# Optimization experiments

Measured on AMD Instinct MI355X. Metric: run time of the kernel, lower is better.

## Reference

```python
import math
import jax, jax.numpy as jnp
import numpy as np

B, S, D_IN, D_OUT = 8, 4096, 512, 512
CHUNK = 64
MAX_LR = 0.2        # config.max_memory_lr
MIN_DECAY = 0.5     # config.min_memory_decay
MAX_NORM = 30.0     # config.memory_max_norm
NORM_EPS = 1e-5     # config.norm_eps (used in normalize_for_delta)


def setup_inputs() -> dict:
    key = jax.random.key(0)
    ks = jax.random.split(key, 5)
    x = jax.random.normal(ks[0], (B, S, D_IN), dtype=jnp.float32)
    # M_init: xavier_uniform(gain=0.1) ~ small; use small normal
    M_init = jax.random.normal(ks[1], (D_OUT, D_IN), dtype=jnp.float32) * 0.02
    # hyperparam projections (Linear(d_in, 1)); torch init: zero weight, logit bias.
    # Use small random weights so the data-dependent path is exercised.
    eta_w = jax.random.normal(ks[2], (1, D_IN), dtype=jnp.float32) * 0.01
    eta_b = jnp.full((1,), math.log(0.08 / 0.92), dtype=jnp.float32)   # inv_sig(memory_lr_init)
    alpha_w = jax.random.normal(ks[3], (1, D_IN), dtype=jnp.float32) * 0.01
    alpha_b = jnp.full((1,), math.log(0.85 / 0.15), dtype=jnp.float32)  # inv_sig(memory_decay_init)
    gate_w = jax.random.normal(ks[4], (1, D_IN), dtype=jnp.float32) * 0.01
    gate_b = jnp.full((1,), 2.0, dtype=jnp.float32)
    return {"x": x, "M_init": M_init, "eta_w": eta_w, "eta_b": eta_b,
            "alpha_w": alpha_w, "alpha_b": alpha_b, "gate_w": gate_w, "gate_b": gate_b}


def _forward(x, M_init, eta_w, eta_b, alpha_w, alpha_b, gate_w, gate_b):
    n_chunks = S // CHUNK
    # [n_chunks, B, C, d_in] for scan over chunks
    xc = x.reshape(B, n_chunks, CHUNK, D_IN).transpose(1, 0, 2, 3)
    M0 = jnp.broadcast_to(M_init, (B, D_OUT, D_IN))

    def step(M, chunk):  # M: [B, d_out, d_in], chunk: [B, C, d_in]
        # per-chunk hyperparams (training mode: base logits = 0)
        eta_tok = jax.nn.sigmoid(chunk @ eta_w.T + eta_b) * MAX_LR            # [B,C,1]
        alpha_tok = MIN_DECAY + jax.nn.sigmoid(chunk @ alpha_w.T + alpha_b) * (1.0 - MIN_DECAY)
        eta = eta_tok.mean(axis=1, keepdims=True)    # [B,1,1]
        alpha = alpha_tok.mean(axis=1, keepdims=True)
        # retrieval: chunk @ M^T
        outputs = jnp.einsum('bcd,bod->bco', chunk, M)  # [B,C,d_out]
        # normalized keys (F.normalize: x / max(||x||, eps))
        kn = jnp.linalg.norm(chunk, axis=-1, keepdims=True)
        keys = chunk / jnp.maximum(kn, NORM_EPS)
        k_mean = keys.mean(axis=1)        # [B,d_in]
        v_target = outputs.mean(axis=1)   # [B,d_out]
        # delta rule rank-1 update
        Mk = jnp.einsum('bod,bd->bo', M, k_mean)
        error = v_target - Mk
        update = error[:, :, None] * k_mean[:, None, :]  # [B,d_out,d_in]
        # chunk_scale = min(C/chunk_size, 1) = 1 here
        M_new = alpha * M + eta * update
        gate = jax.nn.sigmoid(k_mean @ gate_w.T + gate_b)[:, :, None]  # [B,1,1]
        M_new = gate * M_new + (1.0 - gate) * M
        # frobenius-norm clamp
        M_norm = jnp.sqrt(jnp.sum(M_new * M_new, axis=(-2, -1), keepdims=True))
        scale = jnp.minimum(MAX_NORM / (M_norm + 1e-6), 1.0)
        return M_new * scale, outputs

    M_fin, outs = jax.lax.scan(step, M0, xc)  # outs: [n_chunks,B,C,d_out]
    out = outs.transpose(1, 0, 2, 3).reshape(B, S, D_OUT)
    return out, M_fin


def reference(x, M_init, eta_w, eta_b, alpha_w, alpha_b, gate_w, gate_b):
    return _forward(x, M_init, eta_w, eta_b, alpha_w, alpha_b, gate_w, gate_b)
```

## Files before the change

### kernel.cpp

```cpp
#include <hip/hip_runtime.h>
#include <math.h>

#define DIN  512
#define DOUT 512
#define CHK  64
#define NCH  64
#define NB   8
#define SEQ  4096

typedef short bh8_t __attribute__((ext_vector_type(8)));
typedef float f32x4 __attribute__((ext_vector_type(4)));

__device__ __forceinline__ float sigmoidf_(float z){ return 1.0f/(1.0f+__expf(-z)); }

__device__ __forceinline__ unsigned short f2bf(float f){
  unsigned u = __float_as_uint(f);
  unsigned r = (u + 0x7fffu + ((u>>16)&1u)) >> 16;
  return (unsigned short)r;
}
__device__ __forceinline__ void store_bf4(unsigned short* p, float4 v){
  uint2 u;
  u.x = (unsigned)f2bf(v.x) | ((unsigned)f2bf(v.y)<<16);
  u.y = (unsigned)f2bf(v.z) | ((unsigned)f2bf(v.w)<<16);
  *(uint2*)p = u;
}

__global__ __launch_bounds__(256) void k0_m0h(const float* __restrict__ M0, unsigned short* __restrict__ M0h){
  int idx = (blockIdx.x*256 + threadIdx.x)*4;
  float4 v = *(const float4*)(M0+idx);
  store_bf4(M0h+idx, v);
}

__global__ __launch_bounds__(256) void k1_stats(
    const float* __restrict__ x,
    const float* __restrict__ eta_w, const float* __restrict__ eta_b,
    const float* __restrict__ alpha_w, const float* __restrict__ alpha_b,
    const float* __restrict__ gate_w, const float* __restrict__ gate_b,
    float* __restrict__ KM, float* __restrict__ Dv, unsigned short* __restrict__ KMh,
    float* __restrict__ C1, float* __restrict__ C2, float* __restrict__ KM2, float* __restrict__ Q,
    unsigned short* __restrict__ xh)
{
  int j = blockIdx.x, b = blockIdx.y;
  const float* xc = x + ((size_t)b*SEQ + (size_t)j*CHK) * DIN;
  int tid = threadIdx.x;
  int wave = tid >> 6, lane = tid & 63;

  float km_acc[8], xb_acc[8];
#pragma unroll
  for (int k=0;k<8;k++){ km_acc[k]=0.f; xb_acc[k]=0.f; }
  float eta_sum = 0.f, alpha_sum = 0.f;
  float ew[8], aw[8];
#pragma unroll
  for (int k=0;k<8;k++){ ew[k]=eta_w[lane*8+k]; aw[k]=alpha_w[lane*8+k]; }

  for (int tt=0; tt<16; tt++){
    int t = wave*16 + tt;
    const float* xr = xc + (size_t)t*DIN + lane*8;
    float v[8];
#pragma unroll
    for (int k=0;k<8;k++) v[k]=xr[k];
    if (xh){
      uint4 hv;
      hv.x = (unsigned)f2bf(v[0]) | ((unsigned)f2bf(v[1])<<16);
      hv.y = (unsigned)f2bf(v[2]) | ((unsigned)f2bf(v[3])<<16);
      hv.z = (unsigned)f2bf(v[4]) | ((unsigned)f2bf(v[5])<<16);
      hv.w = (unsigned)f2bf(v[6]) | ((unsigned)f2bf(v[7])<<16);
      *(uint4*)&xh[((size_t)b*SEQ + (size_t)j*CHK + t)*DIN + lane*8] = hv;
    }
    float pe=0.f, pa=0.f, pn=0.f;
#pragma unroll
    for (int k=0;k<8;k++){ pe += v[k]*ew[k]; pa += v[k]*aw[k]; pn += v[k]*v[k]; }
#pragma unroll
    for (int off=32; off; off>>=1){
      pe += __shfl_xor(pe, off);
      pa += __shfl_xor(pa, off);
      pn += __shfl_xor(pn, off);
    }
    float inv = 1.0f / fmaxf(sqrtf(pn), 1e-5f);
    eta_sum   += sigmoidf_(pe + eta_b[0]);
    alpha_sum += sigmoidf_(pa + alpha_b[0]);
#pragma unroll
    for (int k=0;k<8;k++){ km_acc[k] += v[k]*inv; xb_acc[k] += v[k]; }
  }

  __shared__ float sKM[4][DIN];
  __shared__ float sXB[4][DIN];
  __shared__ float sEA[4][2];
  __shared__ float sred[4][2];
#pragma unroll
  for (int k=0;k<8;k++){ sKM[wave][lane*8+k]=km_acc[k]; sXB[wave][lane*8+k]=xb_acc[k]; }
  if (lane==0){ sEA[wave][0]=eta_sum; sEA[wave][1]=alpha_sum; }
  __syncthreads();

  float gpart=0.f, km2part=0.f;
  float kmv[2], dvv[2];
#pragma unroll
  for (int k=0;k<2;k++){
    int d = tid*2+k;
    float km = (sKM[0][d]+sKM[1][d]+sKM[2][d]+sKM[3][d]) * (1.0f/64.0f);
    float xb = (sXB[0][d]+sXB[1][d]+sXB[2][d]+sXB[3][d]) * (1.0f/64.0f);
    kmv[k]=km; dvv[k]=xb-km;
    gpart  += km * gate_w[d];
    km2part+= km * km;
  }
#pragma unroll
  for (int off=32; off; off>>=1){
    gpart   += __shfl_xor(gpart, off);
    km2part += __shfl_xor(km2part, off);
  }
  if (lane==0){ sred[wave][0]=gpart; sred[wave][1]=km2part; }
  __syncthreads();

  size_t base = ((size_t)b*NCH + j)*DIN;
#pragma unroll
  for (int k=0;k<2;k++){
    int d = tid*2+k;
    KM[base+d]=kmv[k];
    Dv[base+d]=dvv[k];
    KMh[base+d]=f2bf(kmv[k]);
  }
  if (tid==0){
    float gdot = sred[0][0]+sred[1][0]+sred[2][0]+sred[3][0];
    float km2  = sred[0][1]+sred[1][1]+sred[2][1]+sred[3][1];
    float etam = (sEA[0][0]+sEA[1][0]+sEA[2][0]+sEA[3][0]) * (1.0f/64.0f);
    float alpm = (sEA[0][1]+sEA[1][1]+sEA[2][1]+sEA[3][1]) * (1.0f/64.0f);
    float eta   = 0.2f * etam;
    float alpha = 0.5f + 0.5f * alpm;
    float gate  = sigmoidf_(gdot + gate_b[0]);
    float c1 = gate*alpha + 1.0f - gate;
    float c2 = gate*eta;
    C1[b*NCH+j]  = c1;
    C2[b*NCH+j]  = c2;
    KM2[b*NCH+j] = km2;
    Q[b*NCH+j]   = c2/c1;
  }
}

__global__ __launch_bounds__(256) void k2_g0h0(
    const float* __restrict__ KM, const float* __restrict__ Dv,
    const float* __restrict__ M0, float* __restrict__ G0, float* __restrict__ H0)
{
  int j = blockIdx.x, b = blockIdx.y, half = blockIdx.z;
  __shared__ float sD[DIN], sK[DIN];
  int tid = threadIdx.x;
  size_t base = ((size_t)b*NCH+j)*DIN;
  for (int d=tid; d<DIN; d+=256){ sD[d]=Dv[base+d]; sK[d]=KM[base+d]; }
  __syncthreads();
  int o = half*256 + tid;
  const float* mr = M0 + (size_t)o*DIN;
  float ag=0.f, ah=0.f;
  for (int d=0; d<DIN; d+=4){
    float4 m = *(const float4*)(mr+d);
    ag += m.x*sD[d] + m.y*sD[d+1] + m.z*sD[d+2] + m.w*sD[d+3];
    ah += m.x*sK[d] + m.y*sK[d+1] + m.z*sK[d+2] + m.w*sK[d+3];
  }
  G0[base+o]=ag; H0[base+o]=ah;
}

__global__ __launch_bounds__(512) void k2b_gram(
    const float* __restrict__ KM, const float* __restrict__ Dv,
    const float* __restrict__ Q,
    float* __restrict__ GT, float* __restrict__ WT)
{
  int i = blockIdx.x, b = blockIdx.y;
  __shared__ float sKi[DIN];
  int tid = threadIdx.x;
  const float* kmi = KM + ((size_t)b*NCH+i)*DIN;
  for (int d=tid; d<DIN; d+=512) sKi[d]=kmi[d];
  __syncthreads();
  float qi = Q[b*NCH+i];
  int wave = tid>>6, lane = tid&63;
  for (int j=wave; j<NCH; j+=8){
    const float* dj = Dv + ((size_t)b*NCH+j)*DIN;
    const float* kj = KM + ((size_t)b*NCH+j)*DIN;
    float pd=0.f, pk=0.f;
#pragma unroll
    for (int k=0;k<8;k++){
      int d = lane + k*64;
      pd += sKi[d]*dj[d];
      pk += sKi[d]*kj[d];
    }
#pragma unroll
    for (int off=32; off; off>>=1){ pd += __shfl_xor(pd,off); pk += __shfl_xor(pk,off); }
    if (lane==0){
      GT[((size_t)b*NCH+j)*NCH + i] = qi*pd;
      WT[((size_t)b*NCH+j)*NCH + i] = qi*pk;
    }
  }
}

__global__ __launch_bounds__(64) void k3a_rec(
    const float* __restrict__ G0, const float* __restrict__ H0,
    const float* __restrict__ GT, const float* __restrict__ WT,
    const float* __restrict__ Q,
    float* __restrict__ AU, unsigned short* __restrict__ UQTh, float* __restrict__ DOTS)
{
  int dblk = blockIdx.x, b = blockIdx.y;
  int lane = threadIdx.x;
  int d = dblk*64 + lane;

  __shared__ float sMT[NCH*NCH];
  __shared__ float sWT[NCH*NCH];
  __shared__ float sq[NCH];

  const float4* gt4 = (const float4*)&GT[(size_t)b*NCH*NCH];
  const float4* wt4 = (const float4*)&WT[(size_t)b*NCH*NCH];
#pragma unroll
  for (int t=0;t<16;t++){
    int idx4 = t*64 + lane;
    int idx  = idx4*4;
    int j = idx>>6, i0 = idx&63;
    float4 g = gt4[idx4];
    float4 w = wt4[idx4];
    if (i0+0 >= j){ g.x=0.f; w.x=0.f; }
    if (i0+1 >= j){ g.y=0.f; w.y=0.f; }
    if (i0+2 >= j){ g.z=0.f; w.z=0.f; }
    if (i0+3 >= j){ g.w=0.f; w.w=0.f; }
    *(float4*)&sMT[idx] = g;
    *(float4*)&sWT[idx] = w;
  }
  sq[lane] = Q[b*NCH+lane];
  __syncthreads();

  float au[NCH];
  size_t gb = (size_t)b*NCH*DOUT + d;
#pragma unroll
  for (int j=0;j<NCH;j++) au[j] = G0[gb + (size_t)j*DOUT];

#pragma unroll
  for (int j=1;j<NCH;j++){
    float a = au[j];
    const f32x4* row = (const f32x4*)&sMT[j*64];
    int ng = (j+3)>>2;
#pragma unroll
    for (int g=0; g<ng; g++){
      f32x4 c = row[g];
      a += c[0]*au[g*4+0] + c[1]*au[g*4+1] + c[2]*au[g*4+2] + c[3]*au[g*4+3];
    }
    au[j] = a;
  }
#pragma unroll
  for (int j=0;j<NCH;j++) AU[gb + (size_t)j*DOUT] = au[j];

#pragma unroll
  for (int g=0; g<8; g++){
    uint4 hv;
    hv.x = (unsigned)f2bf(au[g*8+0]*sq[g*8+0]) | ((unsigned)f2bf(au[g*8+1]*sq[g*8+1])<<16);
    hv.y = (unsigned)f2bf(au[g*8+2]*sq[g*8+2]) | ((unsigned)f2bf(au[g*8+3]*sq[g*8+3])<<16);
    hv.z = (unsigned)f2bf(au[g*8+4]*sq[g*8+4]) | ((unsigned)f2bf(au[g*8+5]*sq[g*8+5])<<16);
    hv.w = (unsigned)f2bf(au[g*8+6]*sq[g*8+6]) | ((unsigned)f2bf(au[g*8+7]*sq[g*8+7])<<16);
    *(uint4*)&UQTh[((size_t)b*DOUT + d)*NCH + g*8] = hv;
  }

#pragma unroll
  for (int j=0;j<NCH;j++){
    float w = H0[gb + (size_t)j*DOUT];
    const f32x4* row = (const f32x4*)&sWT[j*64];
    int ng = (j+3)>>2;
#pragma unroll
    for (int g=0; g<ng; g++){
      f32x4 c = row[g];
      w += c[0]*au[g*4+0] + c[1]*au[g*4+1] + c[2]*au[g*4+2] + c[3]*au[g*4+3];
    }
    float s1 = au[j]*w, s2 = au[j]*au[j];
#pragma unroll
    for (int off=32; off; off>>=1){ s1+=__shfl_xor(s1,off); s2+=__shfl_xor(s2,off); }
    if (lane==0){
      DOTS[(((size_t)b*8+dblk)*NCH+j)*2+0] = s1;
      DOTS[(((size_t)b*8+dblk)*NCH+j)*2+1] = s2;
    }
  }
}

__global__ __launch_bounds__(256) void k3b_chain(
    const float* __restrict__ M0, const float* __restrict__ DOTS,
    const float* __restrict__ C1, const float* __restrict__ C2, const float* __restrict__ KM2,
    float* __restrict__ P)
{
  int b = blockIdx.x;
  int tid = threadIdx.x, wave = tid>>6, lane = tid&63;
  __shared__ float sF[4];
  __shared__ float suw[NCH], suu[NCH], sc1[NCH], sc2[NCH], skm2[NCH];

  float f0p = 0.f;
  const float4* m4 = (const float4*)M0;
  for (int i=tid; i<(DOUT*DIN)/4; i+=256){
    float4 v = m4[i];
    f0p += v.x*v.x + v.y*v.y + v.z*v.z + v.w*v.w;
  }
#pragma unroll
  for (int off=32; off; off>>=1) f0p += __shfl_xor(f0p, off);
  if (lane==0) sF[wave]=f0p;

  if (tid < NCH){
    float uw=0.f, uu=0.f;
#pragma unroll
    for (int k=0;k<8;k++){
      uw += DOTS[(((size_t)b*8+k)*NCH+tid)*2+0];
      uu += DOTS[(((size_t)b*8+k)*NCH+tid)*2+1];
    }
    suw[tid]=uw; suu[tid]=uu;
    sc1[tid]=C1[b*NCH+tid]; sc2[tid]=C2[b*NCH+tid]; skm2[tid]=KM2[b*NCH+tid];
  }
  __syncthreads();

  if (tid==0){
    float F = sF[0]+sF[1]+sF[2]+sF[3];
    float p = 1.f;
    P[b*65+0] = 1.f;
    for (int j=0;j<NCH;j++){
      float uw = suw[j], uu = suu[j];
      float c1 = sc1[j], c2 = sc2[j], km2 = skm2[j];
      uw *= p*p; uu *= p*p;
      float Fnew = c1*c1*F + 2.f*c1*c2*uw + c2*c2*uu*km2;
      float scale = fminf(30.0f/(sqrtf(Fnew)+1e-6f), 1.0f);
      F = scale*scale*Fnew;
      p = scale*c1*p;
      P[b*65+j+1] = p;
    }
  }
}

__global__ __launch_bounds__(256) void k4s_s(
    const float* __restrict__ x, const unsigned short* __restrict__ xh,
    const unsigned short* __restrict__ KMh,
    unsigned short* __restrict__ Sh, int use_xh)
{
  int tt = blockIdx.x, b = blockIdx.y;
  int tid = threadIdx.x;
  int lane = tid&63, w = tid>>6, m = lane&15, q = lane>>4;
  __shared__ unsigned short As[64*72];
  __shared__ unsigned short Bs[64*72];
  f32x4 acc[4];
  f32x4 z = {0.f,0.f,0.f,0.f};
#pragma unroll
  for (int nf=0;nf<4;nf++) acc[nf]=z;

  for (int k0=0;k0<DIN;k0+=64){
    uint4 bb[2];
#pragma unroll
    for (int v=0;v<2;v++){
      int idx=v*256+tid; int il=idx>>3, cc=idx&7;
      bb[v] = *(const uint4*)&KMh[((size_t)b*NCH+il)*DIN + k0 + cc*8];
    }
    if (use_xh){
      uint4 av[2];
#pragma unroll
      for (int v=0;v<2;v++){
        int idx=v*256+tid; int row=idx>>3, cc=idx&7;
        av[v] = *(const uint4*)&xh[((size_t)b*SEQ + (size_t)tt*64 + row)*DIN + k0 + cc*8];
      }
      __syncthreads();
#pragma unroll
      for (int v=0;v<2;v++){
        int idx=v*256+tid; int row=idx>>3, cc=idx&7;
        *(uint4*)&As[row*72 + cc*8] = av[v];
      }
    } else {
      float4 xa[4];
#pragma unroll
      for (int v=0;v<4;v++){
        int idx=v*256+tid; int row=idx>>4, cc=idx&15;
        xa[v] = *(const float4*)(x + ((size_t)b*SEQ + (size_t)tt*64 + row)*DIN + k0 + cc*4);
      }
      __syncthreads();
#pragma unroll
      for (int v=0;v<4;v++){
        int idx=v*256+tid; int row=idx>>4, cc=idx&15;
        store_bf4(&As[row*72 + cc*4], xa[v]);
      }
    }
#pragma unroll
    for (int v=0;v<2;v++){
      int idx=v*256+tid; int il=idx>>3, cc=idx&7;
      *(uint4*)&Bs[il*72 + cc*8] = bb[v];
    }
    __syncthreads();
#pragma unroll
    for (int kk=0;kk<2;kk++){
      bh8_t af = *(bh8_t*)&As[(w*16+m)*72 + kk*32 + q*8];
#pragma unroll
      for (int nf=0;nf<4;nf++){
        bh8_t bf_ = *(bh8_t*)&Bs[(nf*16+m)*72 + kk*32 + q*8];
        acc[nf] = __builtin_amdgcn_mfma_f32_16x16x32_bf16(af, bf_, acc[nf], 0,0,0);
      }
    }
  }
  __syncthreads();
  unsigned short* tb = As + w*16*72;
#pragma unroll
  for (int nf=0;nf<4;nf++)
#pragma unroll
    for (int r=0;r<4;r++)
      tb[(q*4+r)*72 + nf*16 + m] = f2bf(acc[nf][r]);
#pragma unroll
  for (int v=0;v<2;v++){
    int idx = v*64 + lane;
    int row = idx>>3, c8 = idx&7;
    uint4 vv = *(uint4*)&tb[row*72 + c8*8];
    *(uint4*)&Sh[((size_t)b*SEQ + (size_t)tt*64 + w*16 + row)*NCH + c8*8] = vv;
  }
}

__global__ __launch_bounds__(256) void k4_out(
    const float* __restrict__ x, const unsigned short* __restrict__ xh,
    const unsigned short* __restrict__ M0h,
    const unsigned short* __restrict__ Sh, const unsigned short* __restrict__ UQTh,
    const float* __restrict__ P, float* __restrict__ out, int use_xh)
{
  int ot = blockIdx.x, j = blockIdx.y, b = blockIdx.z;
  int tid = threadIdx.x;
  int lane = tid&63, w = tid>>6, m = lane&15, q = lane>>4;
  int O0 = ot*128;
  __shared__ __align__(16) char pool[33792];
  unsigned short* As = (unsigned short*)pool;
  unsigned short* Bs = (unsigned short*)pool + 64*72;
  float* ep = (float*)pool;
  f32x4 acc[8];
  f32x4 z = {0.f,0.f,0.f,0.f};
#pragma unroll
  for (int nf=0;nf<8;nf++) acc[nf]=z;
  float p = P[b*65 + j];

  for (int idx=tid; idx<64*64; idx+=256){
    int t = idx>>6, i = idx&63;
    As[t*72+i] = (i<j) ? Sh[((size_t)b*SEQ + (size_t)j*64 + t)*NCH + i] : (unsigned short)0;
  }
#pragma unroll
  for (int v=0; v<4; v++){
    int idx = v*256+tid;
    int ol = idx>>3, cc = idx&7;
    *(uint4*)&Bs[ol*72 + cc*8] = *(const uint4*)&UQTh[((size_t)b*DOUT + O0+ol)*NCH + cc*8];
  }
  __syncthreads();
#pragma unroll
  for (int kk=0;kk<2;kk++){
    bh8_t af = *(bh8_t*)&As[(w*16+m)*72 + kk*32 + q*8];
#pragma unroll
    for (int nf=0;nf<8;nf++){
      bh8_t bf_ = *(bh8_t*)&Bs[(nf*16+m)*72 + kk*32 + q*8];
      acc[nf] = __builtin_amdgcn_mfma_f32_16x16x32_bf16(af, bf_, acc[nf], 0,0,0);
    }
  }

  for (int k0=0;k0<DIN;k0+=64){
    uint4 bb[4];
#pragma unroll
    for (int v=0;v<4;v++){
      int idx=v*256+tid; int ol=idx>>3, cc=idx&7;
      bb[v] = *(const uint4*)&M0h[(size_t)(O0+ol)*DIN + k0 + cc*8];
    }
    if (use_xh){
      uint4 av[2];
#pragma unroll
      for (int v=0;v<2;v++){
        int idx=v*256+tid; int row=idx>>3, cc=idx&7;
        av[v] = *(const uint4*)&xh[((size_t)b*SEQ + (size_t)j*64 + row)*DIN + k0 + cc*8];
      }
      __syncthreads();
#pragma unroll
      for (int v=0;v<2;v++){
        int idx=v*256+tid; int row=idx>>3, cc=idx&7;
        *(uint4*)&As[row*72 + cc*8] = av[v];
      }
    } else {
      float4 xa[4];
#pragma unroll
      for (int v=0;v<4;v++){
        int idx=v*256+tid; int row=idx>>4, cc=idx&15;
        xa[v] = *(const float4*)(x + ((size_t)b*SEQ + (size_t)j*64 + row)*DIN + k0 + cc*4);
      }
      __syncthreads();
#pragma unroll
      for (int v=0;v<4;v++){
        int idx=v*256+tid; int row=idx>>4, cc=idx&15;
        store_bf4(&As[row*72 + cc*4], xa[v]);
      }
    }
#pragma unroll
    for (int v=0;v<4;v++){
      int idx=v*256+tid; int ol=idx>>3, cc=idx&7;
      *(uint4*)&Bs[ol*72 + cc*8] = bb[v];
    }
    __syncthreads();
#pragma unroll
    for (int kk=0;kk<2;kk++){
      bh8_t af = *(bh8_t*)&As[(w*16+m)*72 + kk*32 + q*8];
#pragma unroll
      for (int nf=0;nf<8;nf++){
        bh8_t bf_ = *(bh8_t*)&Bs[(nf*16+m)*72 + kk*32 + q*8];
        acc[nf] = __builtin_amdgcn_mfma_f32_16x16x32_bf16(af, bf_, acc[nf], 0,0,0);
      }
    }
  }

  __syncthreads();
  float* epw = ep + w*16*132;
#pragma unroll
  for (int nf=0;nf<8;nf++)
#pragma unroll
    for (int r=0;r<4;r++)
      epw[(q*4+r)*132 + nf*16 + m] = p*acc[nf][r];
#pragma unroll
  for (int v=0;v<8;v++){
    int idx = v*64 + lane;
    int row = idx>>5, c4 = idx&31;
    float4 vv = *(float4*)&epw[row*132 + c4*4];
    *(float4*)&out[((size_t)b*SEQ + (size_t)j*64 + w*16 + row)*DOUT + O0 + c4*4] = vv;
  }
}

__global__ __launch_bounds__(256) void k5_mfin(
    const float* __restrict__ M0, const float* __restrict__ KM,
    const float* __restrict__ AU, const float* __restrict__ P, const float* __restrict__ Q,
    float* __restrict__ Mout)
{
  int ob = blockIdx.x, b = blockIdx.y;
  int tid = threadIdx.x;
  __shared__ float uo[64][8];
  for (int idx=tid; idx<512; idx+=256){
    int i = idx>>3, oo = idx&7;
    uo[i][oo] = Q[b*NCH+i] * AU[((size_t)b*NCH+i)*DOUT + ob*8+oo];
  }
  __syncthreads();
  float p64 = P[b*65+NCH];
  float acc[2][8];
#pragma unroll
  for (int h=0;h<2;h++)
#pragma unroll
    for (int oo=0;oo<8;oo++) acc[h][oo]=0.f;
  int d0 = tid, d1 = tid+256;
  for (int i=0;i<64;i++){
    float k0 = KM[((size_t)b*NCH+i)*DIN + d0];
    float k1 = KM[((size_t)b*NCH+i)*DIN + d1];
#pragma unroll
    for (int oo=0;oo<8;oo++){
      float u = uo[i][oo];
      acc[0][oo] += u*k0;
      acc[1][oo] += u*k1;
    }
  }
#pragma unroll
  for (int oo=0;oo<8;oo++){
    int o = ob*8+oo;
    Mout[((size_t)b*DOUT + o)*DIN + d0] = p64*(M0[(size_t)o*DIN+d0] + acc[0][oo]);
    Mout[((size_t)b*DOUT + o)*DIN + d1] = p64*(M0[(size_t)o*DIN+d1] + acc[1][oo]);
  }
}

extern "C" void kernel_launch(void* const* d_in, const int* in_sizes, int n_in,
                              void* d_out, int out_size, void* d_ws, size_t ws_size,
                              hipStream_t stream) {
  const float* x       = (const float*)d_in[0];
  const float* M0      = (const float*)d_in[1];
  const float* eta_w   = (const float*)d_in[2];
  const float* eta_b   = (const float*)d_in[3];
  const float* alpha_w = (const float*)d_in[4];
  const float* alpha_b = (const float*)d_in[5];
  const float* gate_w  = (const float*)d_in[6];
  const float* gate_b  = (const float*)d_in[7];
  float* out = (float*)d_out;

  float* ws = (float*)d_ws;
  float* KM   = ws;
  float* Dv   = KM   + 262144;
  float* G0   = Dv   + 262144;
  float* H0   = G0   + 262144;
  float* AU   = H0   + 262144;
  float* GT   = AU   + 262144;
  float* WT   = GT   + 32768;
  float* C1   = WT   + 32768;
  float* C2   = C1   + 512;
  float* KM2  = C2   + 512;
  float* Q    = KM2  + 512;
  float* P    = Q    + 512;
  float* DOTS = P    + 1024;
  unsigned short* M0h  = (unsigned short*)(DOTS + 8192);
  unsigned short* KMh  = M0h  + 262144;
  unsigned short* Sh   = KMh  + 262144;
  unsigned short* UQTh = Sh   + 2097152;
  unsigned short* xh   = UQTh + 262144;

  size_t base_bytes = (size_t)((char*)xh - (char*)d_ws);
  size_t need_xh = base_bytes + (size_t)16777216*2;
  int use_xh = (ws_size >= need_xh) ? 1 : 0;
  unsigned short* xh_arg = use_xh ? xh : (unsigned short*)0;

  k0_m0h<<<dim3(256), 256, 0, stream>>>(M0, M0h);
  k1_stats<<<dim3(NCH, NB), 256, 0, stream>>>(x, eta_w, eta_b, alpha_w, alpha_b,
                                              gate_w, gate_b, KM, Dv, KMh, C1, C2, KM2, Q, xh_arg);
  k2_g0h0<<<dim3(NCH, NB, 2), 256, 0, stream>>>(KM, Dv, M0, G0, H0);
  k2b_gram<<<dim3(NCH, NB), 512, 0, stream>>>(KM, Dv, Q, GT, WT);
  k4s_s<<<dim3(SEQ/64, NB), 256, 0, stream>>>(x, xh, KMh, Sh, use_xh);
  k3a_rec<<<dim3(8, NB), 64, 0, stream>>>(G0, H0, GT, WT, Q, AU, UQTh, DOTS);
  k3b_chain<<<dim3(NB), 256, 0, stream>>>(M0, DOTS, C1, C2, KM2, P);
  k4_out<<<dim3(4, NCH, NB), 256, 0, stream>>>(x, xh, M0h, Sh, UQTh, P, out, use_xh);
  k5_mfin<<<dim3(64, NB), 256, 0, stream>>>(M0, KM, AU, P, Q, out + (size_t)NB*SEQ*DOUT);
}
```

Measured before the change: 498.0 us.

## Enlarge k4_out tile to 256 rows with 2x4 wave grid per block

The output GEMM kernel now has each 512-thread block cover 256 sequence rows (four chunks) by 128 output columns instead of 64 rows. Waves are laid out on a 4x2 grid, each computing a 64x64 sub-tile, so every M0h tile loaded into LDS is reused across four times as many rows. The causal masking of the Sh coefficients moves to per-row bitmasks on vectorized loads, and the per-chunk scale P is chosen per wave row. The aim is to cut redundant M0h traffic and raise MFMA work per LDS load, at the cost of more shared memory, more registers and fewer blocks in the grid (512 instead of 2048).

```diff
diff --git a/kernel.cpp b/kernel.cpp
--- a/kernel.cpp
+++ b/kernel.cpp
@@ -402,111 +402,136 @@
   }
 }
 
-__global__ __launch_bounds__(256) void k4_out(
+__global__ __launch_bounds__(512, 4) void k4_out(
     const float* __restrict__ x, const unsigned short* __restrict__ xh,
     const unsigned short* __restrict__ M0h,
     const unsigned short* __restrict__ Sh, const unsigned short* __restrict__ UQTh,
     const float* __restrict__ P, float* __restrict__ out, int use_xh)
 {
-  int ot = blockIdx.x, j = blockIdx.y, b = blockIdx.z;
+  int ot = blockIdx.x, rb = blockIdx.y, b = blockIdx.z;
   int tid = threadIdx.x;
   int lane = tid&63, w = tid>>6, m = lane&15, q = lane>>4;
+  int wr = w>>1, wc = w&1;
   int O0 = ot*128;
-  __shared__ __align__(16) char pool[33792];
+  int R0 = rb*256;
+
+  __shared__ __align__(16) char pool[55296];
   unsigned short* As = (unsigned short*)pool;
-  unsigned short* Bs = (unsigned short*)pool + 64*72;
+  unsigned short* Bs = (unsigned short*)pool + 256*72;
   float* ep = (float*)pool;
-  f32x4 acc[8];
+
+  f32x4 acc[4][4];
   f32x4 z = {0.f,0.f,0.f,0.f};
 #pragma unroll
-  for (int nf=0;nf<8;nf++) acc[nf]=z;
-  float p = P[b*65 + j];
-
-  for (int idx=tid; idx<64*64; idx+=256){
-    int t = idx>>6, i = idx&63;
-    As[t*72+i] = (i<j) ? Sh[((size_t)b*SEQ + (size_t)j*64 + t)*NCH + i] : (unsigned short)0;
-  }
+  for (int mi=0;mi<4;mi++)
+#pragma unroll
+    for (int nf=0;nf<4;nf++) acc[mi][nf]=z;
+
 #pragma unroll
   for (int v=0; v<4; v++){
-    int idx = v*256+tid;
+    int idx = v*512 + tid;
+    int row = idx>>3, cc = idx&7;
+    int j = (R0 + row)>>6;
+    uint4 sv = *(const uint4*)&Sh[((size_t)b*SEQ + R0 + row)*NCH + cc*8];
+    int i0 = cc*8;
+    unsigned m0 = (i0+0 < j) ? ((i0+1 < j)?0xFFFFFFFFu:0x0000FFFFu) : 0u;
+    unsigned m1 = (i0+2 < j) ? ((i0+3 < j)?0xFFFFFFFFu:0x0000FFFFu) : 0u;
+    unsigned m2 = (i0+4 < j) ? ((i0+5 < j)?0xFFFFFFFFu:0x0000FFFFu) : 0u;
+    unsigned m3 = (i0+6 < j) ? ((i0+7 < j)?0xFFFFFFFFu:0x0000FFFFu) : 0u;
+    sv.x&=m0; sv.y&=m1; sv.z&=m2; sv.w&=m3;
+    *(uint4*)&As[row*72 + cc*8] = sv;
+  }
+#pragma unroll
+  for (int v=0; v<2; v++){
+    int idx = v*512 + tid;
     int ol = idx>>3, cc = idx&7;
     *(uint4*)&Bs[ol*72 + cc*8] = *(const uint4*)&UQTh[((size_t)b*DOUT + O0+ol)*NCH + cc*8];
   }
   __syncthreads();
 #pragma unroll
   for (int kk=0;kk<2;kk++){
-    bh8_t af = *(bh8_t*)&As[(w*16+m)*72 + kk*32 + q*8];
-#pragma unroll
-    for (int nf=0;nf<8;nf++){
-      bh8_t bf_ = *(bh8_t*)&Bs[(nf*16+m)*72 + kk*32 + q*8];
-      acc[nf] = __builtin_amdgcn_mfma_f32_16x16x32_bf16(af, bf_, acc[nf], 0,0,0);
+#pragma unroll
+    for (int mi=0;mi<4;mi++){
+      bh8_t af = *(bh8_t*)&As[(wr*64+mi*16+m)*72 + kk*32 + q*8];
+#pragma unroll
+      for (int nf=0;nf<4;nf++){
+        bh8_t bf_ = *(bh8_t*)&Bs[(wc*64+nf*16+m)*72 + kk*32 + q*8];
+        acc[mi][nf] = __builtin_amdgcn_mfma_f32_16x16x32_bf16(af, bf_, acc[mi][nf], 0,0,0);
+      }
     }
   }
 
   for (int k0=0;k0<DIN;k0+=64){
-    uint4 bb[4];
+    uint4 bb[2];
+#pragma unroll
+    for (int v=0;v<2;v++){
+      int idx=v*512+tid; int ol=idx>>3, cc=idx&7;
+      bb[v] = *(const uint4*)&M0h[(size_t)(O0+ol)*DIN + k0 + cc*8];
+    }
+    if (use_xh){
+      uint4 av[4];
+#pragma unroll
+      for (int v=0;v<4;v++){
+        int idx=v*512+tid; int row=idx>>3, cc=idx&7;
+        av[v] = *(const uint4*)&xh[((size_t)b*SEQ + R0 + row)*DIN + k0 + cc*8];
+      }
+      __syncthreads();
+#pragma unroll
+      for (int v=0;v<4;v++){
+        int idx=v*512+tid; int row=idx>>3, cc=idx&7;
+        *(uint4*)&As[row*72 + cc*8] = av[v];
+      }
+    } else {
+      float4 xa[8];
+#pragma unroll
+      for (int v=0;v<8;v++){
+        int idx=v*512+tid; int row=idx>>4, cc=idx&15;
+        xa[v] = *(const float4*)(x + ((size_t)b*SEQ + R0 + row)*DIN + k0 + cc*4);
+      }
+      __syncthreads();
+#pragma unroll
+      for (int v=0;v<8;v++){
+        int idx=v*512+tid; int row=idx>>4, cc=idx&15;
+        store_bf4(&As[row*72 + cc*4], xa[v]);
+      }
+    }
+#pragma unroll
+    for (int v=0;v<2;v++){
+      int idx=v*512+tid; int ol=idx>>3, cc=idx&7;
+      *(uint4*)&Bs[ol*72 + cc*8] = bb[v];
+    }
+    __syncthreads();
+#pragma unroll
+    for (int kk=0;kk<2;kk++){
+#pragma unroll
+      for (int mi=0;mi<4;mi++){
+        bh8_t af = *(bh8_t*)&As[(wr*64+mi*16+m)*72 + kk*32 + q*8];
+#pragma unroll
+        for (int nf=0;nf<4;nf++){
+          bh8_t bf_ = *(bh8_t*)&Bs[(wc*64+nf*16+m)*72 + kk*32 + q*8];
+          acc[mi][nf] = __builtin_amdgcn_mfma_f32_16x16x32_bf16(af, bf_, acc[mi][nf], 0,0,0);
+        }
+      }
+    }
+  }
+
+  __syncthreads();
+  float p = P[b*65 + rb*4 + wr];
+  float* epw = ep + w*(16*68);
+#pragma unroll
+  for (int mi=0; mi<4; mi++){
+#pragma unroll
+    for (int nf=0;nf<4;nf++)
+#pragma unroll
+      for (int r=0;r<4;r++)
+        epw[(q*4+r)*68 + nf*16 + m] = p*acc[mi][nf][r];
 #pragma unroll
     for (int v=0;v<4;v++){
-      int idx=v*256+tid; int ol=idx>>3, cc=idx&7;
-      bb[v] = *(const uint4*)&M0h[(size_t)(O0+ol)*DIN + k0 + cc*8];
-    }
-    if (use_xh){
-      uint4 av[2];
-#pragma unroll
-      for (int v=0;v<2;v++){
-        int idx=v*256+tid; int row=idx>>3, cc=idx&7;
-        av[v] = *(const uint4*)&xh[((size_t)b*SEQ + (size_t)j*64 + row)*DIN + k0 + cc*8];
-      }
-      __syncthreads();
-#pragma unroll
-      for (int v=0;v<2;v++){
-        int idx=v*256+tid; int row=idx>>3, cc=idx&7;
-        *(uint4*)&As[row*72 + cc*8] = av[v];
-      }
-    } else {
-      float4 xa[4];
-#pragma unroll
-      for (int v=0;v<4;v++){
-        int idx=v*256+tid; int row=idx>>4, cc=idx&15;
-        xa[v] = *(const float4*)(x + ((size_t)b*SEQ + (size_t)j*64 + row)*DIN + k0 + cc*4);
-      }
-      __syncthreads();
-#pragma unroll
-      for (int v=0;v<4;v++){
-        int idx=v*256+tid; int row=idx>>4, cc=idx&15;
-        store_bf4(&As[row*72 + cc*4], xa[v]);
-      }
-    }
-#pragma unroll
-    for (int v=0;v<4;v++){
-      int idx=v*256+tid; int ol=idx>>3, cc=idx&7;
-      *(uint4*)&Bs[ol*72 + cc*8] = bb[v];
-    }
-    __syncthreads();
-#pragma unroll
-    for (int kk=0;kk<2;kk++){
-      bh8_t af = *(bh8_t*)&As[(w*16+m)*72 + kk*32 + q*8];
-#pragma unroll
-      for (int nf=0;nf<8;nf++){
-        bh8_t bf_ = *(bh8_t*)&Bs[(nf*16+m)*72 + kk*32 + q*8];
-        acc[nf] = __builtin_amdgcn_mfma_f32_16x16x32_bf16(af, bf_, acc[nf], 0,0,0);
-      }
-    }
-  }
-
-  __syncthreads();
-  float* epw = ep + w*16*132;
-#pragma unroll
-  for (int nf=0;nf<8;nf++)
-#pragma unroll
-    for (int r=0;r<4;r++)
-      epw[(q*4+r)*132 + nf*16 + m] = p*acc[nf][r];
-#pragma unroll
-  for (int v=0;v<8;v++){
-    int idx = v*64 + lane;
-    int row = idx>>5, c4 = idx&31;
-    float4 vv = *(float4*)&epw[row*132 + c4*4];
-    *(float4*)&out[((size_t)b*SEQ + (size_t)j*64 + w*16 + row)*DOUT + O0 + c4*4] = vv;
+      int idx = v*64 + lane;
+      int row = idx>>4, c4 = idx&15;
+      float4 vv = *(float4*)&epw[row*68 + c4*4];
+      *(float4*)&out[((size_t)b*SEQ + R0 + wr*64 + mi*16 + row)*DOUT + O0 + wc*64 + c4*4] = vv;
+    }
   }
 }
 
@@ -594,6 +619,6 @@
   k4s_s<<<dim3(SEQ/64, NB), 256, 0, stream>>>(x, xh, KMh, Sh, use_xh);
   k3a_rec<<<dim3(8, NB), 64, 0, stream>>>(G0, H0, GT, WT, Q, AU, UQTh, DOTS);
   k3b_chain<<<dim3(NB), 256, 0, stream>>>(M0, DOTS, C1, C2, KM2, P);
-  k4_out<<<dim3(4, NCH, NB), 256, 0, stream>>>(x, xh, M0h, Sh, UQTh, P, out, use_xh);
+  k4_out<<<dim3(4, SEQ/256, NB), 512, 0, stream>>>(x, xh, M0h, Sh, UQTh, P, out, use_xh);
   k5_mfin<<<dim3(64, NB), 256, 0, stream>>>(M0, KM, AU, P, Q, out + (size_t)NB*SEQ*DOUT);
 }
```

Measured after the change: 480.6 us. 1.04x faster.
